# Kernel tuning notes

Hardware: AMD Instinct MI355X
Metric: run time of the kernel (lower is better)

## Reference

```python
import jax, jax.numpy as jnp
import numpy as np

B, L = 2, 8192
HID, HEADS, STATE, K = 1024, 16, 16, 3
HD = HID // HEADS  # head dim = 64


def setup_inputs() -> dict:
    key = jax.random.key(0)
    ks = jax.random.split(key, 4)
    u = jax.random.normal(ks[0], (B, L, 3 * HID), dtype=jnp.float32)
    short_filter_weight = jax.random.normal(ks[1], (3 * HID, 1, K), dtype=jnp.float32)
    log_poles = -jnp.abs(jax.random.normal(ks[2], (1, STATE, 1), dtype=jnp.float32))
    residues = jax.random.normal(ks[3], (1, STATE), dtype=jnp.float32)
    D = jnp.zeros((HID,), dtype=jnp.float32)
    return {"u": u, "short_filter_weight": short_filter_weight,
            "log_poles": log_poles, "residues": residues, "D": D}


def _causal_dconv(x, w):
    # x: (B, C, L), w: (C, 1, K). Cross-correlation (matches torch conv1d)
    # with left pad K-1 == torch padding=K-1 then truncating [..., :L].
    return jax.lax.conv_general_dilated(
        x, w, window_strides=(1,), padding=[(K - 1, 0)],
        dimension_numbers=("NCH", "OIH", "NCH"),
        feature_group_count=x.shape[1])


def _bidir_dconv(x, w):
    # bidirectional FIR: causal conv + anti-causal conv (same filter on the
    # time-reversed signal, reversed back), summed
    fwd = _causal_dconv(x, w)
    rev = _causal_dconv(x[..., ::-1], w)[..., ::-1]
    return fwd + rev


def _fftconv(x, H, fft_size):
    # causal long conv via 2L-point FFT (zero-padded -> linear convolution)
    X = jnp.fft.rfft(x, n=fft_size)
    return jnp.fft.irfft(X * H, n=fft_size)[..., : x.shape[-1]]


def reference(u, short_filter_weight, log_poles, residues, D):
    Bx, Lx, _ = u.shape
    u_t = jnp.transpose(u, (0, 2, 1))                 # (B, 3*HID, L)
    z_pre = _bidir_dconv(u_t, short_filter_weight)    # (B, 3*HID, L)

    # column_split: (B, HEADS, 3*HD, L) -> x2, x1, v each (B, HID, L)
    z = z_pre.reshape(Bx, HEADS, 3 * HD, Lx)
    x2 = z[:, :, :HD].reshape(Bx, HID, Lx)
    x1 = z[:, :, HD:2 * HD].reshape(Bx, HID, Lx)
    v = z[:, :, 2 * HD:].reshape(Bx, HID, Lx)
    x1v = x1 * v

    # implicit long filter from pole/residue parameterization: h (1, 1, L)
    t = jnp.arange(Lx, dtype=jnp.float32)[None, None]           # (1,1,L)
    h = (residues[..., None] * jnp.exp(log_poles * t)).sum(axis=1)[None]

    fft_size = 2 * Lx
    H = jnp.fft.rfft(h.astype(jnp.float32), n=fft_size)          # (1,1,L+1)
    # bidirectional long conv: causal + anti-causal branches
    y = (_fftconv(x1v, H, fft_size)
         + _fftconv(x1v[..., ::-1], H, fft_size)[..., ::-1])

    # skip term and output gate
    y = (y + x1v * D[:, None]) * x2                   # (B, HID, L)
    return jnp.transpose(y, (0, 2, 1))                # (B, L, HID)
```

## Files before the change

kernel.cpp:

```cpp
#include <hip/hip_runtime.h>
#include <cstdint>
#include <cstddef>


#define Bn 2
#define Ln 8192
#define HIDn 1024
#define HEADSn 16
#define STATEn 16
#define THIDn 3072

typedef __attribute__((ext_vector_type(2))) float f32x2;

__device__ __forceinline__ float ldu(const float* __restrict__ base, int t) {
    return ((unsigned)t < (unsigned)Ln) ? base[(size_t)t * THIDn] : 0.0f;
}

template <int CH>
__global__ __launch_bounds__(64, 4) void hyena_phaseA(
    const float* __restrict__ u, const float* __restrict__ sfw,
    const float* __restrict__ lp,
    float* __restrict__ carryF, float* __restrict__ carryG) {
    const int j = threadIdx.x;
    const int chunk = blockIdx.x;
    const int h = blockIdx.y;
    const int b = blockIdx.z;
    const int c1 = h * 192 + 64 + j;
    const int cv = c1 + 64;
    const int t0 = chunk * CH;
    const int t1 = t0 + CH - 1;

    const float* u1 = u + (size_t)b * Ln * THIDn + c1;
    const float* uv = u + (size_t)b * Ln * THIDn + cv;
    const float w10 = sfw[c1 * 3 + 0], w11 = sfw[c1 * 3 + 1], w12 = 2.0f * sfw[c1 * 3 + 2];
    const float wv0 = sfw[cv * 3 + 0], wv1 = sfw[cv * 3 + 1], wv2 = 2.0f * sfw[cv * 3 + 2];

    f32x2 p2[8];
#pragma unroll
    for (int i = 0; i < 8; ++i) p2[i] = (f32x2){expf(lp[2 * i]), expf(lp[2 * i + 1])};

    const int i = h * 64 + j;
    const int gch = b * HIDn + i;
    const size_t base = ((size_t)chunk * (Bn * HIDn) + gch) * 16;

    {
        f32x2 f2[8];
#pragma unroll
        for (int s = 0; s < 8; ++s) f2[s] = (f32x2){0.0f, 0.0f};
        float a0 = ldu(u1, t0 - 2), a1 = ldu(u1, t0 - 1), a2 = ldu(u1, t0), a3 = ldu(u1, t0 + 1);
        float v0 = ldu(uv, t0 - 2), v1 = ldu(uv, t0 - 1), v2 = ldu(uv, t0), v3 = ldu(uv, t0 + 1);
#pragma unroll 8
        for (int tt = 0; tt < CH; ++tt) {
            const int t = t0 + tt;
            const float a4 = ldu(u1, t + 2);
            const float v4 = ldu(uv, t + 2);
            const float z1 = fmaf(w10, a0 + a4, fmaf(w11, a1 + a3, w12 * a2));
            const float zv = fmaf(wv0, v0 + v4, fmaf(wv1, v1 + v3, wv2 * v2));
            const float x = z1 * zv;
            const f32x2 x2 = (f32x2){x, x};
#pragma unroll
            for (int s = 0; s < 8; ++s) f2[s] = __builtin_elementwise_fma(p2[s], f2[s], x2);
            a0 = a1; a1 = a2; a2 = a3; a3 = a4;
            v0 = v1; v1 = v2; v2 = v3; v3 = v4;
        }
        f32x2* cF2 = (f32x2*)(carryF + base);
#pragma unroll
        for (int s = 0; s < 8; ++s) cF2[s] = f2[s];
    }

    {
        f32x2 g2[8];
#pragma unroll
        for (int s = 0; s < 8; ++s) g2[s] = (f32x2){0.0f, 0.0f};
        float a4 = ldu(u1, t1 + 2), a3 = ldu(u1, t1 + 1), a2 = ldu(u1, t1), a1 = ldu(u1, t1 - 1);
        float v4 = ldu(uv, t1 + 2), v3 = ldu(uv, t1 + 1), v2 = ldu(uv, t1), v1 = ldu(uv, t1 - 1);
#pragma unroll 8
        for (int tt = CH - 1; tt >= 0; --tt) {
            const int t = t0 + tt;
            const float a0 = ldu(u1, t - 2);
            const float v0 = ldu(uv, t - 2);
            const float z1 = fmaf(w10, a0 + a4, fmaf(w11, a1 + a3, w12 * a2));
            const float zv = fmaf(wv0, v0 + v4, fmaf(wv1, v1 + v3, wv2 * v2));
            const float x = z1 * zv;
            const f32x2 x2 = (f32x2){x, x};
#pragma unroll
            for (int s = 0; s < 8; ++s) g2[s] = __builtin_elementwise_fma(p2[s], g2[s], x2);
            a4 = a3; a3 = a2; a2 = a1; a1 = a0;
            v4 = v3; v3 = v2; v2 = v1; v1 = v0;
        }
        f32x2* cG2 = (f32x2*)(carryG + base);
#pragma unroll
        for (int s = 0; s < 8; ++s) cG2[s] = g2[s];
    }
}

template <int CH>
__global__ __launch_bounds__(256) void hyena_phaseB(
    const float* __restrict__ lp,
    float* __restrict__ carryF, float* __restrict__ carryG) {
    constexpr int NC = Ln / CH;
    constexpr int UB = 16;
    const int dir = blockIdx.x >> 7;
    const int ht = ((blockIdx.x & 127) << 8) + threadIdx.x;
    const int s = ht & 15;
    const int gch = ht >> 4;
    const float pCH = expf(lp[s] * (float)CH);
    float c = 0.0f;
    if (dir == 0) {
        for (int k0 = 0; k0 < NC; k0 += UB) {
            float loc[UB];
#pragma unroll
            for (int q = 0; q < UB; ++q)
                loc[q] = carryF[((size_t)(k0 + q) * (Bn * HIDn) + gch) * 16 + s];
#pragma unroll
            for (int q = 0; q < UB; ++q) {
                carryF[((size_t)(k0 + q) * (Bn * HIDn) + gch) * 16 + s] = c;
                c = fmaf(pCH, c, loc[q]);
            }
        }
    } else {
        for (int k0 = NC - UB; k0 >= 0; k0 -= UB) {
            float loc[UB];
#pragma unroll
            for (int q = UB - 1; q >= 0; --q)
                loc[q] = carryG[((size_t)(k0 + q) * (Bn * HIDn) + gch) * 16 + s];
#pragma unroll
            for (int q = UB - 1; q >= 0; --q) {
                carryG[((size_t)(k0 + q) * (Bn * HIDn) + gch) * 16 + s] = c;
                c = fmaf(pCH, c, loc[q]);
            }
        }
    }
}

template <int CH>
__global__ __launch_bounds__(64, 4) void hyena_phaseC(
    const float* __restrict__ u, const float* __restrict__ sfw,
    const float* __restrict__ lp, const float* __restrict__ res,
    const float* __restrict__ Dp,
    const float* __restrict__ carryF, const float* __restrict__ carryG,
    float* __restrict__ out) {
    const int j = threadIdx.x;
    const int chunk = blockIdx.x;
    const int h = blockIdx.y;
    const int b = blockIdx.z;
    const int c2 = h * 192 + j;
    const int c1 = c2 + 64;
    const int cv = c2 + 128;
    const int i = h * 64 + j;
    const int gch = b * HIDn + i;
    const int t0 = chunk * CH;
    const int t1 = t0 + CH - 1;

    const float* u2 = u + (size_t)b * Ln * THIDn + c2;
    const float* u1 = u + (size_t)b * Ln * THIDn + c1;
    const float* uv = u + (size_t)b * Ln * THIDn + cv;
    float* op = out + (size_t)b * Ln * HIDn + i;
    const float w20 = sfw[c2 * 3 + 0], w21 = sfw[c2 * 3 + 1], w22 = 2.0f * sfw[c2 * 3 + 2];
    const float w10 = sfw[c1 * 3 + 0], w11 = sfw[c1 * 3 + 1], w12 = 2.0f * sfw[c1 * 3 + 2];
    const float wv0 = sfw[cv * 3 + 0], wv1 = sfw[cv * 3 + 1], wv2 = 2.0f * sfw[cv * 3 + 2];

    f32x2 p2[8];
#pragma unroll
    for (int s = 0; s < 8; ++s) p2[s] = (f32x2){expf(lp[2 * s]), expf(lp[2 * s + 1])};
    float rr[STATEn];
#pragma unroll
    for (int s = 0; s < STATEn; ++s) rr[s] = res[s];

    const size_t cbase = ((size_t)chunk * (Bn * HIDn) + gch) * 16;

    {
        f32x2 f2[8];
        const f32x2* cF2 = (const f32x2*)(carryF + cbase);
#pragma unroll
        for (int s = 0; s < 8; ++s) f2[s] = cF2[s];
        float a0 = ldu(u1, t0 - 2), a1 = ldu(u1, t0 - 1), a2 = ldu(u1, t0), a3 = ldu(u1, t0 + 1);
        float v0 = ldu(uv, t0 - 2), v1 = ldu(uv, t0 - 1), v2 = ldu(uv, t0), v3 = ldu(uv, t0 + 1);
#pragma unroll 8
        for (int tt = 0; tt < CH; ++tt) {
            const int t = t0 + tt;
            const float a4 = ldu(u1, t + 2);
            const float v4 = ldu(uv, t + 2);
            const float z1 = fmaf(w10, a0 + a4, fmaf(w11, a1 + a3, w12 * a2));
            const float zv = fmaf(wv0, v0 + v4, fmaf(wv1, v1 + v3, wv2 * v2));
            const float x = z1 * zv;
            const f32x2 xb = (f32x2){x, x};
#pragma unroll
            for (int s = 0; s < 8; ++s) f2[s] = __builtin_elementwise_fma(p2[s], f2[s], xb);
            float acc0 = rr[0] * f2[0].x, acc1 = rr[1] * f2[0].y;
            float acc2 = rr[2] * f2[1].x, acc3 = rr[3] * f2[1].y;
#pragma unroll
            for (int s = 2; s < 8; s += 2) {
                acc0 = fmaf(rr[2 * s + 0], f2[s].x, acc0);
                acc1 = fmaf(rr[2 * s + 1], f2[s].y, acc1);
                acc2 = fmaf(rr[2 * s + 2], f2[s + 1].x, acc2);
                acc3 = fmaf(rr[2 * s + 3], f2[s + 1].y, acc3);
            }
            op[(size_t)t * HIDn] = (acc0 + acc1) + (acc2 + acc3);
            a0 = a1; a1 = a2; a2 = a3; a3 = a4;
            v0 = v1; v1 = v2; v2 = v3; v3 = v4;
        }
    }

    {
        f32x2 g2[8];
        const f32x2* cG2 = (const f32x2*)(carryG + cbase);
#pragma unroll
        for (int s = 0; s < 8; ++s) g2[s] = cG2[s];
        const float dI = Dp[i];
        float a4 = ldu(u1, t1 + 2), a3 = ldu(u1, t1 + 1), a2 = ldu(u1, t1), a1 = ldu(u1, t1 - 1);
        float v4 = ldu(uv, t1 + 2), v3 = ldu(uv, t1 + 1), v2 = ldu(uv, t1), v1 = ldu(uv, t1 - 1);
        float e4 = ldu(u2, t1 + 2), e3 = ldu(u2, t1 + 1), e2 = ldu(u2, t1), e1 = ldu(u2, t1 - 1);
#pragma unroll 8
        for (int tt = CH - 1; tt >= 0; --tt) {
            const int t = t0 + tt;
            const float yc = op[(size_t)t * HIDn];
            const float a0 = ldu(u1, t - 2);
            const float v0 = ldu(uv, t - 2);
            const float e0 = ldu(u2, t - 2);
            const float z1 = fmaf(w10, a0 + a4, fmaf(w11, a1 + a3, w12 * a2));
            const float zv = fmaf(wv0, v0 + v4, fmaf(wv1, v1 + v3, wv2 * v2));
            const float z2 = fmaf(w20, e0 + e4, fmaf(w21, e1 + e3, w22 * e2));
            const float x = z1 * zv;
            const f32x2 xb = (f32x2){x, x};
#pragma unroll
            for (int s = 0; s < 8; ++s) g2[s] = __builtin_elementwise_fma(p2[s], g2[s], xb);
            float acc0 = rr[0] * g2[0].x, acc1 = rr[1] * g2[0].y;
            float acc2 = rr[2] * g2[1].x, acc3 = rr[3] * g2[1].y;
#pragma unroll
            for (int s = 2; s < 8; s += 2) {
                acc0 = fmaf(rr[2 * s + 0], g2[s].x, acc0);
                acc1 = fmaf(rr[2 * s + 1], g2[s].y, acc1);
                acc2 = fmaf(rr[2 * s + 2], g2[s + 1].x, acc2);
                acc3 = fmaf(rr[2 * s + 3], g2[s + 1].y, acc3);
            }
            const float ya = (acc0 + acc1) + (acc2 + acc3);
            op[(size_t)t * HIDn] = (yc + ya + dI * x) * z2;
            a4 = a3; a3 = a2; a2 = a1; a1 = a0;
            v4 = v3; v3 = v2; v2 = v1; v1 = v0;
            e4 = e3; e3 = e2; e2 = e1; e1 = e0;
        }
    }
}

template <int CH>
static void run_all(const float* u, const float* sfw, const float* lp,
                    const float* res, const float* Dp, float* out,
                    void* ws, hipStream_t stream) {
    constexpr int NC = Ln / CH;
    float* carryF = (float*)ws;
    float* carryG = carryF + (size_t)NC * (Bn * HIDn) * 16;
    dim3 grid(NC, HEADSn, Bn);
    hipLaunchKernelGGL((hyena_phaseA<CH>), grid, dim3(64), 0, stream,
                       u, sfw, lp, carryF, carryG);
    hipLaunchKernelGGL((hyena_phaseB<CH>), dim3(256), dim3(256), 0, stream,
                       lp, carryF, carryG);
    hipLaunchKernelGGL((hyena_phaseC<CH>), grid, dim3(64), 0, stream,
                       u, sfw, lp, res, Dp, carryF, carryG, out);
}

extern "C" void kernel_launch(void* const* d_in, const int* in_sizes, int n_in,
                              void* d_out, int out_size, void* d_ws, size_t ws_size,
                              hipStream_t stream) {
    const float* u   = (const float*)d_in[0];
    const float* sfw = (const float*)d_in[1];
    const float* lp  = (const float*)d_in[2];
    const float* res = (const float*)d_in[3];
    const float* Dp  = (const float*)d_in[4];
    float* out = (float*)d_out;

    const size_t need64 = ((size_t)1 << 31) / 64;
    if (ws_size >= need64)            run_all<64>(u, sfw, lp, res, Dp, out, d_ws, stream);
    else if (ws_size >= need64 / 2)   run_all<128>(u, sfw, lp, res, Dp, out, d_ws, stream);
    else if (ws_size >= need64 / 4)   run_all<256>(u, sfw, lp, res, Dp, out, d_ws, stream);
    else                              run_all<512>(u, sfw, lp, res, Dp, out, d_ws, stream);
}
```

Before: 415.5 us.

## Specialize interior chunks without bounds checks, reorder grid, shrink chunk size

Splits phase A and C bodies into templates so interior chunks skip the per-element bounds checks on the input loads. The grid is reordered to put heads and batch in the fast dimensions, the occupancy hint is raised to 8 blocks, and the residue reduction uses packed f32x2 FMAs. The preferred chunk length drops from 64 to 32 when workspace allows, which gives more blocks but doubles the carry traffic and the serial phase B length.

```diff
diff --git a/kernel.cpp b/kernel.cpp
--- a/kernel.cpp
+++ b/kernel.cpp
@@ -12,23 +12,82 @@
 
 typedef __attribute__((ext_vector_type(2))) float f32x2;
 
+template <bool G>
 __device__ __forceinline__ float ldu(const float* __restrict__ base, int t) {
-    return ((unsigned)t < (unsigned)Ln) ? base[(size_t)t * THIDn] : 0.0f;
+    if constexpr (G)
+        return ((unsigned)t < (unsigned)Ln) ? base[(size_t)t * THIDn] : 0.0f;
+    else
+        return base[(size_t)t * THIDn];
+}
+
+template <int CH, bool G>
+__device__ __forceinline__ void phaseA_body(
+    const float* __restrict__ u1, const float* __restrict__ uv,
+    float w10, float w11, float w12, float wv0, float wv1, float wv2,
+    const f32x2* __restrict__ p2, int t0,
+    f32x2* __restrict__ cF2, f32x2* __restrict__ cG2) {
+    const int t1 = t0 + CH - 1;
+    {
+        f32x2 f2[8];
+#pragma unroll
+        for (int s = 0; s < 8; ++s) f2[s] = (f32x2){0.0f, 0.0f};
+        float a0 = ldu<G>(u1, t0 - 2), a1 = ldu<G>(u1, t0 - 1), a2 = ldu<G>(u1, t0), a3 = ldu<G>(u1, t0 + 1);
+        float v0 = ldu<G>(uv, t0 - 2), v1 = ldu<G>(uv, t0 - 1), v2 = ldu<G>(uv, t0), v3 = ldu<G>(uv, t0 + 1);
+#pragma unroll 8
+        for (int tt = 0; tt < CH; ++tt) {
+            const int t = t0 + tt;
+            const float a4 = ldu<G>(u1, t + 2);
+            const float v4 = ldu<G>(uv, t + 2);
+            const float z1 = fmaf(w10, a0 + a4, fmaf(w11, a1 + a3, w12 * a2));
+            const float zv = fmaf(wv0, v0 + v4, fmaf(wv1, v1 + v3, wv2 * v2));
+            const float x = z1 * zv;
+            const f32x2 xb = (f32x2){x, x};
+#pragma unroll
+            for (int s = 0; s < 8; ++s) f2[s] = __builtin_elementwise_fma(p2[s], f2[s], xb);
+            a0 = a1; a1 = a2; a2 = a3; a3 = a4;
+            v0 = v1; v1 = v2; v2 = v3; v3 = v4;
+        }
+#pragma unroll
+        for (int s = 0; s < 8; ++s) cF2[s] = f2[s];
+    }
+    {
+        f32x2 g2[8];
+#pragma unroll
+        for (int s = 0; s < 8; ++s) g2[s] = (f32x2){0.0f, 0.0f};
+        float a4 = ldu<G>(u1, t1 + 2), a3 = ldu<G>(u1, t1 + 1), a2 = ldu<G>(u1, t1), a1 = ldu<G>(u1, t1 - 1);
+        float v4 = ldu<G>(uv, t1 + 2), v3 = ldu<G>(uv, t1 + 1), v2 = ldu<G>(uv, t1), v1 = ldu<G>(uv, t1 - 1);
+#pragma unroll 8
+        for (int tt = CH - 1; tt >= 0; --tt) {
+            const int t = t0 + tt;
+            const float a0 = ldu<G>(u1, t - 2);
+            const float v0 = ldu<G>(uv, t - 2);
+            const float z1 = fmaf(w10, a0 + a4, fmaf(w11, a1 + a3, w12 * a2));
+            const float zv = fmaf(wv0, v0 + v4, fmaf(wv1, v1 + v3, wv2 * v2));
+            const float x = z1 * zv;
+            const f32x2 xb = (f32x2){x, x};
+#pragma unroll
+            for (int s = 0; s < 8; ++s) g2[s] = __builtin_elementwise_fma(p2[s], g2[s], xb);
+            a4 = a3; a3 = a2; a2 = a1; a1 = a0;
+            v4 = v3; v3 = v2; v2 = v1; v1 = v0;
+        }
+#pragma unroll
+        for (int s = 0; s < 8; ++s) cG2[s] = g2[s];
+    }
 }
 
 template <int CH>
-__global__ __launch_bounds__(64, 4) void hyena_phaseA(
+__global__ __launch_bounds__(64, 8) void hyena_phaseA(
     const float* __restrict__ u, const float* __restrict__ sfw,
     const float* __restrict__ lp,
     float* __restrict__ carryF, float* __restrict__ carryG) {
+    constexpr int NC = Ln / CH;
     const int j = threadIdx.x;
-    const int chunk = blockIdx.x;
-    const int h = blockIdx.y;
-    const int b = blockIdx.z;
+    const int h = blockIdx.x;
+    const int b = blockIdx.y;
+    const int chunk = blockIdx.z;
     const int c1 = h * 192 + 64 + j;
     const int cv = c1 + 64;
     const int t0 = chunk * CH;
-    const int t1 = t0 + CH - 1;
 
     const float* u1 = u + (size_t)b * Ln * THIDn + c1;
     const float* uv = u + (size_t)b * Ln * THIDn + cv;
@@ -37,61 +96,17 @@
 
     f32x2 p2[8];
 #pragma unroll
-    for (int i = 0; i < 8; ++i) p2[i] = (f32x2){expf(lp[2 * i]), expf(lp[2 * i + 1])};
-
-    const int i = h * 64 + j;
-    const int gch = b * HIDn + i;
+    for (int s = 0; s < 8; ++s) p2[s] = (f32x2){expf(lp[2 * s]), expf(lp[2 * s + 1])};
+
+    const int gch = b * HIDn + h * 64 + j;
     const size_t base = ((size_t)chunk * (Bn * HIDn) + gch) * 16;
-
-    {
-        f32x2 f2[8];
-#pragma unroll
-        for (int s = 0; s < 8; ++s) f2[s] = (f32x2){0.0f, 0.0f};
-        float a0 = ldu(u1, t0 - 2), a1 = ldu(u1, t0 - 1), a2 = ldu(u1, t0), a3 = ldu(u1, t0 + 1);
-        float v0 = ldu(uv, t0 - 2), v1 = ldu(uv, t0 - 1), v2 = ldu(uv, t0), v3 = ldu(uv, t0 + 1);
-#pragma unroll 8
-        for (int tt = 0; tt < CH; ++tt) {
-            const int t = t0 + tt;
-            const float a4 = ldu(u1, t + 2);
-            const float v4 = ldu(uv, t + 2);
-            const float z1 = fmaf(w10, a0 + a4, fmaf(w11, a1 + a3, w12 * a2));
-            const float zv = fmaf(wv0, v0 + v4, fmaf(wv1, v1 + v3, wv2 * v2));
-            const float x = z1 * zv;
-            const f32x2 x2 = (f32x2){x, x};
-#pragma unroll
-            for (int s = 0; s < 8; ++s) f2[s] = __builtin_elementwise_fma(p2[s], f2[s], x2);
-            a0 = a1; a1 = a2; a2 = a3; a3 = a4;
-            v0 = v1; v1 = v2; v2 = v3; v3 = v4;
-        }
-        f32x2* cF2 = (f32x2*)(carryF + base);
-#pragma unroll
-        for (int s = 0; s < 8; ++s) cF2[s] = f2[s];
-    }
-
-    {
-        f32x2 g2[8];
-#pragma unroll
-        for (int s = 0; s < 8; ++s) g2[s] = (f32x2){0.0f, 0.0f};
-        float a4 = ldu(u1, t1 + 2), a3 = ldu(u1, t1 + 1), a2 = ldu(u1, t1), a1 = ldu(u1, t1 - 1);
-        float v4 = ldu(uv, t1 + 2), v3 = ldu(uv, t1 + 1), v2 = ldu(uv, t1), v1 = ldu(uv, t1 - 1);
-#pragma unroll 8
-        for (int tt = CH - 1; tt >= 0; --tt) {
-            const int t = t0 + tt;
-            const float a0 = ldu(u1, t - 2);
-            const float v0 = ldu(uv, t - 2);
-            const float z1 = fmaf(w10, a0 + a4, fmaf(w11, a1 + a3, w12 * a2));
-            const float zv = fmaf(wv0, v0 + v4, fmaf(wv1, v1 + v3, wv2 * v2));
-            const float x = z1 * zv;
-            const f32x2 x2 = (f32x2){x, x};
-#pragma unroll
-            for (int s = 0; s < 8; ++s) g2[s] = __builtin_elementwise_fma(p2[s], g2[s], x2);
-            a4 = a3; a3 = a2; a2 = a1; a1 = a0;
-            v4 = v3; v3 = v2; v2 = v1; v1 = v0;
-        }
-        f32x2* cG2 = (f32x2*)(carryG + base);
-#pragma unroll
-        for (int s = 0; s < 8; ++s) cG2[s] = g2[s];
-    }
+    f32x2* cF2 = (f32x2*)(carryF + base);
+    f32x2* cG2 = (f32x2*)(carryG + base);
+
+    if (chunk > 0 && chunk < NC - 1)
+        phaseA_body<CH, false>(u1, uv, w10, w11, w12, wv0, wv1, wv2, p2, t0, cF2, cG2);
+    else
+        phaseA_body<CH, true>(u1, uv, w10, w11, w12, wv0, wv1, wv2, p2, t0, cF2, cG2);
 }
 
 template <int CH>
@@ -133,24 +148,100 @@
     }
 }
 
+template <int CH, bool G>
+__device__ __forceinline__ void phaseC_body(
+    const float* __restrict__ u2, const float* __restrict__ u1,
+    const float* __restrict__ uv, float* __restrict__ op,
+    float w20, float w21, float w22, float w10, float w11, float w12,
+    float wv0, float wv1, float wv2,
+    const f32x2* __restrict__ p2, const f32x2* __restrict__ rr2,
+    float dI, int t0,
+    const f32x2* __restrict__ cF2, const f32x2* __restrict__ cG2) {
+    const int t1 = t0 + CH - 1;
+    {
+        f32x2 f2[8];
+#pragma unroll
+        for (int s = 0; s < 8; ++s) f2[s] = cF2[s];
+        float a0 = ldu<G>(u1, t0 - 2), a1 = ldu<G>(u1, t0 - 1), a2 = ldu<G>(u1, t0), a3 = ldu<G>(u1, t0 + 1);
+        float v0 = ldu<G>(uv, t0 - 2), v1 = ldu<G>(uv, t0 - 1), v2 = ldu<G>(uv, t0), v3 = ldu<G>(uv, t0 + 1);
+#pragma unroll 8
+        for (int tt = 0; tt < CH; ++tt) {
+            const int t = t0 + tt;
+            const float a4 = ldu<G>(u1, t + 2);
+            const float v4 = ldu<G>(uv, t + 2);
+            const float z1 = fmaf(w10, a0 + a4, fmaf(w11, a1 + a3, w12 * a2));
+            const float zv = fmaf(wv0, v0 + v4, fmaf(wv1, v1 + v3, wv2 * v2));
+            const float x = z1 * zv;
+            const f32x2 xb = (f32x2){x, x};
+#pragma unroll
+            for (int s = 0; s < 8; ++s) f2[s] = __builtin_elementwise_fma(p2[s], f2[s], xb);
+            f32x2 acc0 = rr2[0] * f2[0], acc1 = rr2[1] * f2[1];
+            f32x2 acc2 = rr2[2] * f2[2], acc3 = rr2[3] * f2[3];
+            acc0 = __builtin_elementwise_fma(rr2[4], f2[4], acc0);
+            acc1 = __builtin_elementwise_fma(rr2[5], f2[5], acc1);
+            acc2 = __builtin_elementwise_fma(rr2[6], f2[6], acc2);
+            acc3 = __builtin_elementwise_fma(rr2[7], f2[7], acc3);
+            const f32x2 sum = (acc0 + acc1) + (acc2 + acc3);
+            op[(size_t)t * HIDn] = sum.x + sum.y;
+            a0 = a1; a1 = a2; a2 = a3; a3 = a4;
+            v0 = v1; v1 = v2; v2 = v3; v3 = v4;
+        }
+    }
+    {
+        f32x2 g2[8];
+#pragma unroll
+        for (int s = 0; s < 8; ++s) g2[s] = cG2[s];
+        float a4 = ldu<G>(u1, t1 + 2), a3 = ldu<G>(u1, t1 + 1), a2 = ldu<G>(u1, t1), a1 = ldu<G>(u1, t1 - 1);
+        float v4 = ldu<G>(uv, t1 + 2), v3 = ldu<G>(uv, t1 + 1), v2 = ldu<G>(uv, t1), v1 = ldu<G>(uv, t1 - 1);
+        float e4 = ldu<G>(u2, t1 + 2), e3 = ldu<G>(u2, t1 + 1), e2 = ldu<G>(u2, t1), e1 = ldu<G>(u2, t1 - 1);
+#pragma unroll 8
+        for (int tt = CH - 1; tt >= 0; --tt) {
+            const int t = t0 + tt;
+            const float yc = op[(size_t)t * HIDn];
+            const float a0 = ldu<G>(u1, t - 2);
+            const float v0 = ldu<G>(uv, t - 2);
+            const float e0 = ldu<G>(u2, t - 2);
+            const float z1 = fmaf(w10, a0 + a4, fmaf(w11, a1 + a3, w12 * a2));
+            const float zv = fmaf(wv0, v0 + v4, fmaf(wv1, v1 + v3, wv2 * v2));
+            const float z2 = fmaf(w20, e0 + e4, fmaf(w21, e1 + e3, w22 * e2));
+            const float x = z1 * zv;
+            const f32x2 xb = (f32x2){x, x};
+#pragma unroll
+            for (int s = 0; s < 8; ++s) g2[s] = __builtin_elementwise_fma(p2[s], g2[s], xb);
+            f32x2 acc0 = rr2[0] * g2[0], acc1 = rr2[1] * g2[1];
+            f32x2 acc2 = rr2[2] * g2[2], acc3 = rr2[3] * g2[3];
+            acc0 = __builtin_elementwise_fma(rr2[4], g2[4], acc0);
+            acc1 = __builtin_elementwise_fma(rr2[5], g2[5], acc1);
+            acc2 = __builtin_elementwise_fma(rr2[6], g2[6], acc2);
+            acc3 = __builtin_elementwise_fma(rr2[7], g2[7], acc3);
+            const f32x2 sum = (acc0 + acc1) + (acc2 + acc3);
+            const float ya = sum.x + sum.y;
+            op[(size_t)t * HIDn] = (yc + ya + dI * x) * z2;
+            a4 = a3; a3 = a2; a2 = a1; a1 = a0;
+            v4 = v3; v3 = v2; v2 = v1; v1 = v0;
+            e4 = e3; e3 = e2; e2 = e1; e1 = e0;
+        }
+    }
+}
+
 template <int CH>
-__global__ __launch_bounds__(64, 4) void hyena_phaseC(
+__global__ __launch_bounds__(64, 8) void hyena_phaseC(
     const float* __restrict__ u, const float* __restrict__ sfw,
     const float* __restrict__ lp, const float* __restrict__ res,
     const float* __restrict__ Dp,
     const float* __restrict__ carryF, const float* __restrict__ carryG,
     float* __restrict__ out) {
+    constexpr int NC = Ln / CH;
     const int j = threadIdx.x;
-    const int chunk = blockIdx.x;
-    const int h = blockIdx.y;
-    const int b = blockIdx.z;
+    const int h = blockIdx.x;
+    const int b = blockIdx.y;
+    const int chunk = blockIdx.z;
     const int c2 = h * 192 + j;
     const int c1 = c2 + 64;
     const int cv = c2 + 128;
     const int i = h * 64 + j;
     const int gch = b * HIDn + i;
     const int t0 = chunk * CH;
-    const int t1 = t0 + CH - 1;
 
     const float* u2 = u + (size_t)b * Ln * THIDn + c2;
     const float* u1 = u + (size_t)b * Ln * THIDn + c1;
@@ -160,87 +251,23 @@
     const float w10 = sfw[c1 * 3 + 0], w11 = sfw[c1 * 3 + 1], w12 = 2.0f * sfw[c1 * 3 + 2];
     const float wv0 = sfw[cv * 3 + 0], wv1 = sfw[cv * 3 + 1], wv2 = 2.0f * sfw[cv * 3 + 2];
 
-    f32x2 p2[8];
+    f32x2 p2[8], rr2[8];
 #pragma unroll
     for (int s = 0; s < 8; ++s) p2[s] = (f32x2){expf(lp[2 * s]), expf(lp[2 * s + 1])};
-    float rr[STATEn];
-#pragma unroll
-    for (int s = 0; s < STATEn; ++s) rr[s] = res[s];
+#pragma unroll
+    for (int s = 0; s < 8; ++s) rr2[s] = (f32x2){res[2 * s], res[2 * s + 1]};
+    const float dI = Dp[i];
 
     const size_t cbase = ((size_t)chunk * (Bn * HIDn) + gch) * 16;
-
-    {
-        f32x2 f2[8];
-        const f32x2* cF2 = (const f32x2*)(carryF + cbase);
-#pragma unroll
-        for (int s = 0; s < 8; ++s) f2[s] = cF2[s];
-        float a0 = ldu(u1, t0 - 2), a1 = ldu(u1, t0 - 1), a2 = ldu(u1, t0), a3 = ldu(u1, t0 + 1);
-        float v0 = ldu(uv, t0 - 2), v1 = ldu(uv, t0 - 1), v2 = ldu(uv, t0), v3 = ldu(uv, t0 + 1);
-#pragma unroll 8
-        for (int tt = 0; tt < CH; ++tt) {
-            const int t = t0 + tt;
-            const float a4 = ldu(u1, t + 2);
-            const float v4 = ldu(uv, t + 2);
-            const float z1 = fmaf(w10, a0 + a4, fmaf(w11, a1 + a3, w12 * a2));
-            const float zv = fmaf(wv0, v0 + v4, fmaf(wv1, v1 + v3, wv2 * v2));
-            const float x = z1 * zv;
-            const f32x2 xb = (f32x2){x, x};
-#pragma unroll
-            for (int s = 0; s < 8; ++s) f2[s] = __builtin_elementwise_fma(p2[s], f2[s], xb);
-            float acc0 = rr[0] * f2[0].x, acc1 = rr[1] * f2[0].y;
-            float acc2 = rr[2] * f2[1].x, acc3 = rr[3] * f2[1].y;
-#pragma unroll
-            for (int s = 2; s < 8; s += 2) {
-                acc0 = fmaf(rr[2 * s + 0], f2[s].x, acc0);
-                acc1 = fmaf(rr[2 * s + 1], f2[s].y, acc1);
-                acc2 = fmaf(rr[2 * s + 2], f2[s + 1].x, acc2);
-                acc3 = fmaf(rr[2 * s + 3], f2[s + 1].y, acc3);
-            }
-            op[(size_t)t * HIDn] = (acc0 + acc1) + (acc2 + acc3);
-            a0 = a1; a1 = a2; a2 = a3; a3 = a4;
-            v0 = v1; v1 = v2; v2 = v3; v3 = v4;
-        }
-    }
-
-    {
-        f32x2 g2[8];
-        const f32x2* cG2 = (const f32x2*)(carryG + cbase);
-#pragma unroll
-        for (int s = 0; s < 8; ++s) g2[s] = cG2[s];
-        const float dI = Dp[i];
-        float a4 = ldu(u1, t1 + 2), a3 = ldu(u1, t1 + 1), a2 = ldu(u1, t1), a1 = ldu(u1, t1 - 1);
-        float v4 = ldu(uv, t1 + 2), v3 = ldu(uv, t1 + 1), v2 = ldu(uv, t1), v1 = ldu(uv, t1 - 1);
-        float e4 = ldu(u2, t1 + 2), e3 = ldu(u2, t1 + 1), e2 = ldu(u2, t1), e1 = ldu(u2, t1 - 1);
-#pragma unroll 8
-        for (int tt = CH - 1; tt >= 0; --tt) {
-            const int t = t0 + tt;
-            const float yc = op[(size_t)t * HIDn];
-            const float a0 = ldu(u1, t - 2);
-            const float v0 = ldu(uv, t - 2);
-            const float e0 = ldu(u2, t - 2);
-            const float z1 = fmaf(w10, a0 + a4, fmaf(w11, a1 + a3, w12 * a2));
-            const float zv = fmaf(wv0, v0 + v4, fmaf(wv1, v1 + v3, wv2 * v2));
-            const float z2 = fmaf(w20, e0 + e4, fmaf(w21, e1 + e3, w22 * e2));
-            const float x = z1 * zv;
-            const f32x2 xb = (f32x2){x, x};
-#pragma unroll
-            for (int s = 0; s < 8; ++s) g2[s] = __builtin_elementwise_fma(p2[s], g2[s], xb);
-            float acc0 = rr[0] * g2[0].x, acc1 = rr[1] * g2[0].y;
-            float acc2 = rr[2] * g2[1].x, acc3 = rr[3] * g2[1].y;
-#pragma unroll
-            for (int s = 2; s < 8; s += 2) {
-                acc0 = fmaf(rr[2 * s + 0], g2[s].x, acc0);
-                acc1 = fmaf(rr[2 * s + 1], g2[s].y, acc1);
-                acc2 = fmaf(rr[2 * s + 2], g2[s + 1].x, acc2);
-                acc3 = fmaf(rr[2 * s + 3], g2[s + 1].y, acc3);
-            }
-            const float ya = (acc0 + acc1) + (acc2 + acc3);
-            op[(size_t)t * HIDn] = (yc + ya + dI * x) * z2;
-            a4 = a3; a3 = a2; a2 = a1; a1 = a0;
-            v4 = v3; v3 = v2; v2 = v1; v1 = v0;
-            e4 = e3; e3 = e2; e2 = e1; e1 = e0;
-        }
-    }
+    const f32x2* cF2 = (const f32x2*)(carryF + cbase);
+    const f32x2* cG2 = (const f32x2*)(carryG + cbase);
+
+    if (chunk > 0 && chunk < NC - 1)
+        phaseC_body<CH, false>(u2, u1, uv, op, w20, w21, w22, w10, w11, w12,
+                               wv0, wv1, wv2, p2, rr2, dI, t0, cF2, cG2);
+    else
+        phaseC_body<CH, true>(u2, u1, uv, op, w20, w21, w22, w10, w11, w12,
+                              wv0, wv1, wv2, p2, rr2, dI, t0, cF2, cG2);
 }
 
 template <int CH>
@@ -250,7 +277,7 @@
     constexpr int NC = Ln / CH;
     float* carryF = (float*)ws;
     float* carryG = carryF + (size_t)NC * (Bn * HIDn) * 16;
-    dim3 grid(NC, HEADSn, Bn);
+    dim3 grid(HEADSn, Bn, NC);
     hipLaunchKernelGGL((hyena_phaseA<CH>), grid, dim3(64), 0, stream,
                        u, sfw, lp, carryF, carryG);
     hipLaunchKernelGGL((hyena_phaseB<CH>), dim3(256), dim3(256), 0, stream,
@@ -269,9 +296,9 @@
     const float* Dp  = (const float*)d_in[4];
     float* out = (float*)d_out;
 
-    const size_t need64 = ((size_t)1 << 31) / 64;
-    if (ws_size >= need64)            run_all<64>(u, sfw, lp, res, Dp, out, d_ws, stream);
-    else if (ws_size >= need64 / 2)   run_all<128>(u, sfw, lp, res, Dp, out, d_ws, stream);
-    else if (ws_size >= need64 / 4)   run_all<256>(u, sfw, lp, res, Dp, out, d_ws, stream);
-    else                              run_all<512>(u, sfw, lp, res, Dp, out, d_ws, stream);
-}
+    const size_t need32 = ((size_t)1 << 31) / 32;
+    if (ws_size >= need32)            run_all<32>(u, sfw, lp, res, Dp, out, d_ws, stream);
+    else if (ws_size >= need32 / 2)   run_all<64>(u, sfw, lp, res, Dp, out, d_ws, stream);
+    else if (ws_size >= need32 / 4)   run_all<128>(u, sfw, lp, res, Dp, out, d_ws, stream);
+    else                              run_all<256>(u, sfw, lp, res, Dp, out, d_ws, stream);
+}
```

Result: slower. 644.8 us (+55.2%).
